# Kernel optimization log

Measured on AMD Instinct MI355X. Metric: run time of the kernel, lower is better.

## Reference

```python
import jax, jax.numpy as jnp
import numpy as np

BLOCK_SIZE = 128  # init_kwargs block_size


def setup_inputs() -> dict:
    key = jax.random.key(0)
    kq, kk, kv = jax.random.split(key, 3)
    shape = (8, 16, 4096, 128)  # [B, H, L, D]
    q = jax.random.normal(kq, shape, dtype=jnp.float32)
    k = jax.random.normal(kk, shape, dtype=jnp.float32)
    v = jax.random.normal(kv, shape, dtype=jnp.float32)
    return {"q": q, "k": k, "v": v}


def reference(q, k, v):
    # Block-diagonal local attention. The torch code builds a dense [L,L]
    # score matrix filled with -10000 off the block diagonal; exp(-10000)
    # underflows to exactly 0 in fp32 after max-subtraction, so the dense
    # softmax is mathematically identical to per-block softmax. We honor
    # the block sparsity and never materialize the L x L matrix.
    w = BLOCK_SIZE
    B, H, L, D = q.shape
    nb = L // w
    qb = q.reshape(B, H, nb, w, D)
    kb = k.reshape(B, H, nb, w, D)
    vb = v.reshape(B, H, nb, w, D)
    # NOTE: original applies NO 1/sqrt(D) scaling.
    score = jnp.einsum('bhnwd,bhnud->bhnwu', qb, kb)   # [B,H,nb,w,w]
    probs = jax.nn.softmax(score, axis=-1)
    out = jnp.einsum('bhnwu,bhnud->bhnwd', probs, vb)
    return out.reshape(B, H, L, D)
```

## Files before the change

kernel.cpp:

```cpp
#include <hip/hip_runtime.h>

typedef _Float16 half8  __attribute__((ext_vector_type(8)));
typedef _Float16 half4v __attribute__((ext_vector_type(4)));
typedef _Float16 half2v __attribute__((ext_vector_type(2)));
typedef float    f32x4  __attribute__((ext_vector_type(4)));

__device__ __forceinline__ int swz(int row) {
    return ((row ^ (row >> 3)) & 15) << 4;
}

__global__ __launch_bounds__(512, 4) void battn_kernel(
    const float* __restrict__ Q, const float* __restrict__ K,
    const float* __restrict__ V, float* __restrict__ O)
{
    extern __shared__ __align__(16) char smem[];
    const int tid  = threadIdx.x;
    const int lane = tid & 63;
    const int w    = tid >> 6;
    const int la   = lane & 15;
    const int u    = lane >> 4;
    const size_t base = (size_t)blockIdx.x * (128 * 128);

    const float* Qb = Q + base;
    const float* Kb = K + base;
    const float* Vb = V + base;
    float*       Ob = O + base;

    float4 kreg[8];
#pragma unroll
    for (int it = 0; it < 8; ++it) {
        const int idx = it * 2048 + tid * 4;
        kreg[it] = *(const float4*)(Kb + idx);
    }
    float4 vreg[2][4];
#pragma unroll
    for (int it = 0; it < 2; ++it) {
        const int tau = it * 512 + tid;
        const int d0 = (tau & 15) * 8;
        const int j0 = (tau >> 4) * 2;
        vreg[it][0] = *(const float4*)(Vb + j0 * 128 + d0);
        vreg[it][1] = *(const float4*)(Vb + j0 * 128 + d0 + 4);
        vreg[it][2] = *(const float4*)(Vb + (j0 + 1) * 128 + d0);
        vreg[it][3] = *(const float4*)(Vb + (j0 + 1) * 128 + d0 + 4);
    }
    half8 qfrag[4];
    {
        const float* qrow = Qb + (w * 16 + la) * 128;
#pragma unroll
        for (int kk = 0; kk < 4; ++kk) {
            const float4 a = *(const float4*)(qrow + kk * 32 + u * 8);
            const float4 b = *(const float4*)(qrow + kk * 32 + u * 8 + 4);
            qfrag[kk][0] = (_Float16)a.x; qfrag[kk][1] = (_Float16)a.y;
            qfrag[kk][2] = (_Float16)a.z; qfrag[kk][3] = (_Float16)a.w;
            qfrag[kk][4] = (_Float16)b.x; qfrag[kk][5] = (_Float16)b.y;
            qfrag[kk][6] = (_Float16)b.z; qfrag[kk][7] = (_Float16)b.w;
        }
    }
#pragma unroll
    for (int it = 0; it < 8; ++it) {
        const int idx = it * 2048 + tid * 4;
        const int row = idx >> 7;
        const int col = idx & 127;
        half4v h;
        h[0] = (_Float16)kreg[it].x; h[1] = (_Float16)kreg[it].y;
        h[2] = (_Float16)kreg[it].z; h[3] = (_Float16)kreg[it].w;
        int byte = row * 256 + col * 2;
        byte ^= swz(row);
        *(half4v*)(smem + byte) = h;
    }
#pragma unroll
    for (int it = 0; it < 2; ++it) {
        const int tau = it * 512 + tid;
        const int d0 = (tau & 15) * 8;
        const int j0 = (tau >> 4) * 2;
        const float r0[8] = {vreg[it][0].x, vreg[it][0].y, vreg[it][0].z, vreg[it][0].w,
                             vreg[it][1].x, vreg[it][1].y, vreg[it][1].z, vreg[it][1].w};
        const float r1[8] = {vreg[it][2].x, vreg[it][2].y, vreg[it][2].z, vreg[it][2].w,
                             vreg[it][3].x, vreg[it][3].y, vreg[it][3].z, vreg[it][3].w};
#pragma unroll
        for (int i = 0; i < 8; ++i) {
            half2v h;
            h[0] = (_Float16)r0[i];
            h[1] = (_Float16)r1[i];
            const int row = d0 + i;
            int byte = 32768 + row * 256 + j0 * 2;
            byte ^= swz(row);
            *(half2v*)(smem + byte) = h;
        }
    }
    __syncthreads();

    f32x4 acc[8];
#pragma unroll
    for (int t = 0; t < 8; ++t) acc[t] = (f32x4){0.f, 0.f, 0.f, 0.f};
#pragma unroll
    for (int t = 0; t < 8; ++t) {
#pragma unroll
        for (int kk = 0; kk < 4; ++kk) {
            const int row = t * 16 + la;
            int byte = row * 256 + kk * 64 + u * 16;
            byte ^= swz(row);
            const half8 kf = *(const half8*)(smem + byte);
            acc[t] = __builtin_amdgcn_mfma_f32_16x16x32_f16(qfrag[kk], kf, acc[t], 0, 0, 0);
        }
    }

    float inv[4];
#pragma unroll
    for (int r = 0; r < 4; ++r) {
        float m = acc[0][r];
#pragma unroll
        for (int t = 1; t < 8; ++t) m = fmaxf(m, acc[t][r]);
        m = fmaxf(m, __shfl_xor(m, 1));
        m = fmaxf(m, __shfl_xor(m, 2));
        m = fmaxf(m, __shfl_xor(m, 4));
        m = fmaxf(m, __shfl_xor(m, 8));
        float s = 0.f;
#pragma unroll
        for (int t = 0; t < 8; ++t) {
            const float e = __expf(acc[t][r] - m);
            acc[t][r] = e;
            s += e;
        }
        s += __shfl_xor(s, 1);
        s += __shfl_xor(s, 2);
        s += __shfl_xor(s, 4);
        s += __shfl_xor(s, 8);
        inv[r] = 1.0f / s;
    }

    __syncthreads();

#pragma unroll
    for (int t = 0; t < 8; ++t) {
#pragma unroll
        for (int r = 0; r < 4; ++r) {
            const int row = u * 4 + r;
            const int col = t * 16 + la;
            int byte = w * 4096 + row * 256 + col * 2;
            byte ^= swz(row);
            *(_Float16*)(smem + byte) = (_Float16)(acc[t][r] * inv[r]);
        }
    }
    __syncthreads();

    half8 pb[4];
#pragma unroll
    for (int kk = 0; kk < 4; ++kk) {
        int byte = w * 4096 + la * 256 + kk * 64 + u * 16;
        byte ^= swz(la);
        pb[kk] = *(const half8*)(smem + byte);
    }
    f32x4 oacc[8];
#pragma unroll
    for (int tt = 0; tt < 8; ++tt) oacc[tt] = (f32x4){0.f, 0.f, 0.f, 0.f};
#pragma unroll
    for (int tt = 0; tt < 8; ++tt) {
#pragma unroll
        for (int kk = 0; kk < 4; ++kk) {
            const int row = tt * 16 + la;
            int byte = 32768 + row * 256 + kk * 64 + u * 16;
            byte ^= swz(row);
            const half8 vf = *(const half8*)(smem + byte);
            oacc[tt] = __builtin_amdgcn_mfma_f32_16x16x32_f16(vf, pb[kk], oacc[tt], 0, 0, 0);
        }
    }
#pragma unroll
    for (int tt = 0; tt < 8; ++tt) {
        const float4 ov = make_float4(oacc[tt][0], oacc[tt][1], oacc[tt][2], oacc[tt][3]);
        *(float4*)(Ob + (w * 16 + la) * 128 + tt * 16 + u * 4) = ov;
    }
}

extern "C" void kernel_launch(void* const* d_in, const int* in_sizes, int n_in,
                              void* d_out, int out_size, void* d_ws, size_t ws_size,
                              hipStream_t stream) {
    const float* q = (const float*)d_in[0];
    const float* k = (const float*)d_in[1];
    const float* v = (const float*)d_in[2];
    float* o = (float*)d_out;
    const int nblocks = in_sizes[0] / (128 * 128);
    battn_kernel<<<dim3(nblocks), dim3(512), 65536, stream>>>(q, k, v, o);
}
```

Before: 211.1 us.

## Transpose QK^T MFMA layout and pass probabilities via lane shuffles instead of LDS

```diff
diff --git a/kernel.cpp b/kernel.cpp
--- a/kernel.cpp
+++ b/kernel.cpp
@@ -13,7 +13,7 @@
     const float* __restrict__ Q, const float* __restrict__ K,
     const float* __restrict__ V, float* __restrict__ O)
 {
-    extern __shared__ __align__(16) char smem[];
+    __shared__ __align__(16) char smem[65536];
     const int tid  = threadIdx.x;
     const int lane = tid & 63;
     const int w    = tid >> 6;
@@ -28,10 +28,9 @@
 
     float4 kreg[8];
 #pragma unroll
-    for (int it = 0; it < 8; ++it) {
-        const int idx = it * 2048 + tid * 4;
-        kreg[it] = *(const float4*)(Kb + idx);
-    }
+    for (int it = 0; it < 8; ++it)
+        kreg[it] = *(const float4*)(Kb + it * 2048 + tid * 4);
+
     float4 vreg[2][4];
 #pragma unroll
     for (int it = 0; it < 2; ++it) {
@@ -101,74 +100,64 @@
             int byte = row * 256 + kk * 64 + u * 16;
             byte ^= swz(row);
             const half8 kf = *(const half8*)(smem + byte);
-            acc[t] = __builtin_amdgcn_mfma_f32_16x16x32_f16(qfrag[kk], kf, acc[t], 0, 0, 0);
+            acc[t] = __builtin_amdgcn_mfma_f32_16x16x32_f16(kf, qfrag[kk], acc[t], 0, 0, 0);
         }
     }
 
-    float inv[4];
+    float m = acc[0][0];
 #pragma unroll
-    for (int r = 0; r < 4; ++r) {
-        float m = acc[0][r];
+    for (int t = 0; t < 8; ++t)
 #pragma unroll
-        for (int t = 1; t < 8; ++t) m = fmaxf(m, acc[t][r]);
-        m = fmaxf(m, __shfl_xor(m, 1));
-        m = fmaxf(m, __shfl_xor(m, 2));
-        m = fmaxf(m, __shfl_xor(m, 4));
-        m = fmaxf(m, __shfl_xor(m, 8));
-        float s = 0.f;
+        for (int r = 0; r < 4; ++r) m = fmaxf(m, acc[t][r]);
+    m = fmaxf(m, __shfl_xor(m, 16));
+    m = fmaxf(m, __shfl_xor(m, 32));
+    float s = 0.f;
 #pragma unroll
-        for (int t = 0; t < 8; ++t) {
+    for (int t = 0; t < 8; ++t)
+#pragma unroll
+        for (int r = 0; r < 4; ++r) {
             const float e = __expf(acc[t][r] - m);
             acc[t][r] = e;
             s += e;
         }
-        s += __shfl_xor(s, 1);
-        s += __shfl_xor(s, 2);
-        s += __shfl_xor(s, 4);
-        s += __shfl_xor(s, 8);
-        inv[r] = 1.0f / s;
+    s += __shfl_xor(s, 16);
+    s += __shfl_xor(s, 32);
+    const float inv = 1.0f / s;
+#pragma unroll
+    for (int t = 0; t < 8; ++t)
+#pragma unroll
+        for (int r = 0; r < 4; ++r) acc[t][r] *= inv;
+
+    const int srcA = la + 32 * (u & 1);
+    const int srcB = srcA + 16;
+    const int hi   = u >> 1;
+    half8 pa[4];
+#pragma unroll
+    for (int kk = 0; kk < 4; ++kk) {
+#pragma unroll
+        for (int r = 0; r < 4; ++r) {
+            const float sA0 = __shfl(acc[2 * kk][r],     srcA);
+            const float sA1 = __shfl(acc[2 * kk + 1][r], srcA);
+            const float sB0 = __shfl(acc[2 * kk][r],     srcB);
+            const float sB1 = __shfl(acc[2 * kk + 1][r], srcB);
+            pa[kk][r]     = (_Float16)(hi ? sA1 : sA0);
+            pa[kk][4 + r] = (_Float16)(hi ? sB1 : sB0);
+        }
     }
 
-    __syncthreads();
-
 #pragma unroll
-    for (int t = 0; t < 8; ++t) {
-#pragma unroll
-        for (int r = 0; r < 4; ++r) {
-            const int row = u * 4 + r;
-            const int col = t * 16 + la;
-            int byte = w * 4096 + row * 256 + col * 2;
-            byte ^= swz(row);
-            *(_Float16*)(smem + byte) = (_Float16)(acc[t][r] * inv[r]);
-        }
-    }
-    __syncthreads();
-
-    half8 pb[4];
-#pragma unroll
-    for (int kk = 0; kk < 4; ++kk) {
-        int byte = w * 4096 + la * 256 + kk * 64 + u * 16;
-        byte ^= swz(la);
-        pb[kk] = *(const half8*)(smem + byte);
-    }
-    f32x4 oacc[8];
-#pragma unroll
-    for (int tt = 0; tt < 8; ++tt) oacc[tt] = (f32x4){0.f, 0.f, 0.f, 0.f};
-#pragma unroll
-    for (int tt = 0; tt < 8; ++tt) {
+    for (int dt = 0; dt < 8; ++dt) {
+        f32x4 oa = (f32x4){0.f, 0.f, 0.f, 0.f};
 #pragma unroll
         for (int kk = 0; kk < 4; ++kk) {
-            const int row = tt * 16 + la;
+            const int row = dt * 16 + la;
             int byte = 32768 + row * 256 + kk * 64 + u * 16;
             byte ^= swz(row);
             const half8 vf = *(const half8*)(smem + byte);
-            oacc[tt] = __builtin_amdgcn_mfma_f32_16x16x32_f16(vf, pb[kk], oacc[tt], 0, 0, 0);
+            oa = __builtin_amdgcn_mfma_f32_16x16x32_f16(vf, pa[kk], oa, 0, 0, 0);
         }
-    }
-#pragma unroll
-    for (int tt = 0; tt < 8; ++tt) {
-        const float4 ov = make_float4(oacc[tt][0], oacc[tt][1], oacc[tt][2], oacc[tt][3]);
-        *(float4*)(Ob + (w * 16 + la) * 128 + tt * 16 + u * 4) = ov;
+        *(float4*)(Ob + (w * 16 + la) * 128 + dt * 16 + u * 4) =
+            make_float4(oa[0], oa[1], oa[2], oa[3]);
     }
 }
 
@@ -180,5 +169,5 @@
     const float* v = (const float*)d_in[2];
     float* o = (float*)d_out;
     const int nblocks = in_sizes[0] / (128 * 128);
-    battn_kernel<<<dim3(nblocks), dim3(512), 65536, stream>>>(q, k, v, o);
+    battn_kernel<<<dim3(nblocks), dim3(512), 0, stream>>>(q, k, v, o);
 }
```

New measurement: 210.8 us, median of 2. About the same (-0.2%).
